# Performance work log

Measured on AMD Instinct MI355X. Metric: run time of the kernel, lower is better.

Reference implementation:

```python
import jax, jax.numpy as jnp
import numpy as np

MIN_NORM = 1e-15
EPS = 1e-7
MASK_FILL = -9e15


def logmap0(x, c):
    # Hyperboloid log map at the origin (HGCN convention, K = 1/c)
    K = 1.0 / c
    sqrtK = K ** 0.5
    y = x[:, 1:]
    y_norm = jnp.clip(jnp.linalg.norm(y, axis=-1, keepdims=True), MIN_NORM)
    theta = jnp.clip(x[:, :1] / sqrtK, 1.0 + EPS)
    res = sqrtK * jnp.arccosh(theta) * y / y_norm
    return jnp.concatenate([jnp.zeros_like(x[:, :1]), res], axis=1)


def proj(x, c):
    # normalize: recompute time coordinate so x lies on the hyperboloid
    K = 1.0 / c
    y = x[:, 1:]
    x0 = jnp.sqrt(K + jnp.sum(y * y, axis=-1, keepdims=True))
    return jnp.concatenate([x0, y], axis=1)


def expmap0(u, c):
    K = 1.0 / c
    sqrtK = K ** 0.5
    x = u[:, 1:]
    x_norm = jnp.clip(jnp.linalg.norm(x, axis=-1, keepdims=True), MIN_NORM)
    theta = x_norm / sqrtK
    res = jnp.concatenate(
        [sqrtK * jnp.cosh(theta), sqrtK * jnp.sinh(theta) * x / x_norm], axis=1
    )
    return proj(res, c)


def setup_inputs() -> dict:
    key = jax.random.key(0)
    k1, k2, k3, k4, k5 = jax.random.split(key, 5)
    N, D_in, D_out = 8192, 256, 256
    x = jax.random.normal(k1, (N, D_in), dtype=jnp.float32)
    adj = jax.random.randint(k2, (N, N), 0, 2, dtype=jnp.int32)
    W_gcn = jax.random.normal(k3, (D_in - 1, D_out - 1), dtype=jnp.float32)
    # xavier_uniform-like scale (gain=1.414)
    std_w = 1.414 * (2.0 / (D_out + D_out)) ** 0.5
    W_att = jax.random.normal(k4, (D_out, D_out), dtype=jnp.float32) * std_w
    std_a = 1.414 * (2.0 / (2 * D_out + 1)) ** 0.5
    a_att = jax.random.normal(k5, (2 * D_out, 1), dtype=jnp.float32) * std_a
    return {"x": x, "adj": adj, "k": 1, "W_gcn": W_gcn, "W_att": W_att, "a_att": a_att}


def reference(x, adj, k, W_gcn, W_att, a_att):
    c = float(k)  # curvature
    N = x.shape[0]
    # tangent-space linear map, keeping time coordinate zero
    logx = logmap0(x, c)
    Wx = logx[:, 1:] @ W_gcn  # [N, D_out-1]
    tmp = jnp.concatenate([jnp.zeros((N, 1), x.dtype), Wx], axis=1)
    fun7 = proj(expmap0(tmp, c), c)  # expmap0 + normalize
    h_in = logmap0(fun7, c)  # [N, D_out]
    # GraphAttentionLayer (dense GAT; a_input @ a decomposes into rank-1 terms)
    h = h_in @ W_att  # [N, F]
    F_ = h.shape[1]
    e = (h @ a_att[:F_]) + (h @ a_att[F_:]).T  # [N, N]; == cat([h_i, h_j]) @ a
    att = jnp.where(adj > 0, e, MASK_FILL)
    att = jax.nn.softmax(att, axis=1)  # dropout omitted (eval mode)
    h_prime = att @ h
    emb = jax.nn.elu(h_prime)  # concat=True
    emb = proj(emb, c)  # manifold.normalize
    # HypAct with sigmoid
    out = expmap0(jax.nn.sigmoid(logmap0(emb, c)), c)
    return out
```

## Files before the change

kernel.cpp:

```cpp
#include <hip/hip_runtime.h>
#include <hip/hip_bf16.h>
#include <math.h>

typedef __attribute__((ext_vector_type(4))) float f32x4;
typedef __attribute__((ext_vector_type(8))) short bf16x8;
typedef __attribute__((ext_vector_type(2))) unsigned long long u64x2;

#define N_ROWS 8192
#define D 256
#define MSHIFT 16.0f
#define NKB 8
#define KRANGE (N_ROWS / NKB)
#define NSTEP (KRANGE / 32)

__device__ __forceinline__ unsigned short f2bf(float f) {
    unsigned int u = __float_as_uint(f);
    unsigned int r = u + 0x7FFFu + ((u >> 16) & 1u);
    return (unsigned short)(r >> 16);
}
__device__ __forceinline__ float bf2f(unsigned short h) {
    return __uint_as_float(((unsigned int)h) << 16);
}

__device__ __forceinline__ float breduce_sum256(float v, float* sb) {
#pragma unroll
    for (int off = 32; off; off >>= 1) v += __shfl_down(v, off);
    int wid = threadIdx.x >> 6;
    __syncthreads();
    if ((threadIdx.x & 63) == 0) sb[wid] = v;
    __syncthreads();
    return sb[0] + sb[1] + sb[2] + sb[3];
}

__device__ __forceinline__ void dma16(const void* g, void* l) {
    __builtin_amdgcn_global_load_lds(
        (const __attribute__((address_space(1))) unsigned int*)g,
        (__attribute__((address_space(3))) unsigned int*)l, 16, 0, 0);
}

__device__ __forceinline__ bf16x8 bits2bf(unsigned int w32, int sh) {
    unsigned int m = w32 >> sh;
    bf16x8 r;
#pragma unroll
    for (int j = 0; j < 8; ++j)
        r[j] = (m & (1u << j)) ? (short)0x3F80 : (short)0;
    return r;
}

__global__ void __launch_bounds__(512)
k_pack(const int* __restrict__ adj, const float* __restrict__ wexp,
       unsigned long long* __restrict__ pack64, float* __restrict__ rowsum) {
    __shared__ float wlds[N_ROWS];
    const int tid = threadIdx.x;
    const int l = tid & 63;
    const int row = blockIdx.x * 8 + (tid >> 6);
#pragma unroll
    for (int i = 0; i < 4; ++i) {
        float4 v4 = *(const float4*)(wexp + (i * 512 + tid) * 4);
        *(float4*)(&wlds[(i * 512 + tid) * 4]) = v4;
    }
    __syncthreads();

    const int* arow = adj + (size_t)row * N_ROWS;
    float rs = 0.f;
    for (int g = 0; g < 8; ++g) {
        int a[16];
#pragma unroll
        for (int i = 0; i < 16; ++i) a[i] = arow[(g * 16 + i) * 64 + l];
        __builtin_amdgcn_sched_barrier(0);
        unsigned long long m[16];
#pragma unroll
        for (int i = 0; i < 16; ++i) {
            m[i] = __ballot(a[i] != 0);
            rs += a[i] ? wlds[(g * 16 + i) * 64 + l] : 0.f;
        }
        if (l == 0) {
#pragma unroll
            for (int i = 0; i < 8; ++i) {
                u64x2 st = {m[2 * i], m[2 * i + 1]};
                *(u64x2*)(&pack64[(size_t)row * 128 + g * 16 + 2 * i]) = st;
            }
        }
    }
#pragma unroll
    for (int off = 32; off; off >>= 1) rs += __shfl_xor(rs, off);
    if (l == 0) rowsum[row] = rs;
}

__global__ void k_M2v(const float* __restrict__ Wg, const float* __restrict__ Wa,
                      const float* __restrict__ aatt,
                      unsigned short* __restrict__ M2Thi, unsigned short* __restrict__ M2Tlo,
                      float* __restrict__ v) {
    __shared__ float sb[4];
    int k = blockIdx.x, t = threadIdx.x;
    float acc = 0.f;
#pragma unroll 8
    for (int m = 0; m < 255; ++m)
        acc += Wg[k * 255 + m] * Wa[(m + 1) * 256 + t];
    unsigned short hi = f2bf(acc);
    unsigned short lo = f2bf(acc - bf2f(hi));
    M2Thi[t * 256 + k] = hi;
    M2Tlo[t * 256 + k] = lo;
    if (k == 0) { M2Thi[t * 256 + 255] = 0; M2Tlo[t * 256 + 255] = 0; }
    float s = breduce_sum256(acc * aatt[256 + t], sb);
    if (t == 0) v[k] = s;
}

__global__ void k_logw(const float* __restrict__ x, const float* __restrict__ v,
                       float* __restrict__ wexp,
                       unsigned short* __restrict__ Awhi, unsigned short* __restrict__ Awlo) {
    __shared__ float sb[4];
    int i0 = blockIdx.x * 8, t = threadIdx.x;
    float vv = (t >= 1) ? v[t - 1] : 0.f;
#pragma unroll
    for (int r = 0; r < 8; ++r) {
        float xv = x[(size_t)(i0 + r) * D + t];
        float yv = (t >= 1) ? xv : 0.f;
        float ss = breduce_sum256(yv * yv, sb);
        float x0 = x[(size_t)(i0 + r) * D];
        float coef = acoshf(fmaxf(x0, 1.f + 1e-7f)) / fmaxf(sqrtf(ss), 1e-15f);
        float lg = coef * yv;
        float c = breduce_sum256(lg * vv, sb);
        float w = expf(c - MSHIFT);
        if (t == r) wexp[i0 + r] = w;
        float aw = w * lg;
        unsigned short hi = f2bf(aw);
        unsigned short lo = f2bf(aw - bf2f(hi));
        int kd = (t == 0) ? 255 : (t - 1);
        Awhi[(size_t)(i0 + r) * 256 + kd] = hi;
        Awlo[(size_t)(i0 + r) * 256 + kd] = lo;
    }
}

__global__ void __launch_bounds__(512)
k_hGT(const unsigned short* __restrict__ M2Thi, const unsigned short* __restrict__ M2Tlo,
      const unsigned short* __restrict__ Awhi, const unsigned short* __restrict__ Awlo,
      unsigned short* __restrict__ GT) {
    __shared__ __align__(16) char ahi[32768], alo[32768], bhi[8192], blo[8192];
    const int tid = threadIdx.x;
    const int w = tid >> 6, l = tid & 63;
    const int lr = l & 15, lq = l >> 4;
    const int i0 = blockIdx.x * 64;
    const int gs = (l & 7) ^ (l >> 3);

    const unsigned short* srcAhi[4];
    const unsigned short* srcAlo[4];
#pragma unroll
    for (int i = 0; i < 4; ++i) {
        int rowA = (w * 4 + i) * 8 + (l >> 3);
        srcAhi[i] = M2Thi + rowA * 256 + gs * 8;
        srcAlo[i] = M2Tlo + rowA * 256 + gs * 8;
    }
    int rowB = w * 8 + (l >> 3);
    const unsigned short* srcBhi = Awhi + (size_t)(i0 + rowB) * 256 + gs * 8;
    const unsigned short* srcBlo = Awlo + (size_t)(i0 + rowB) * 256 + gs * 8;

    f32x4 zero4 = {0.f, 0.f, 0.f, 0.f};
    f32x4 acc[2][4];
#pragma unroll
    for (int m = 0; m < 2; ++m)
#pragma unroll
        for (int n = 0; n < 4; ++n) acc[m][n] = zero4;

    for (int t = 0; t < 4; ++t) {
        if (t) __syncthreads();
#pragma unroll
        for (int i = 0; i < 4; ++i) {
            dma16(srcAhi[i] + t * 64, ahi + (w * 4 + i) * 1024);
            dma16(srcAlo[i] + t * 64, alo + (w * 4 + i) * 1024);
        }
        dma16(srcBhi + t * 64, bhi + w * 1024);
        dma16(srcBlo + t * 64, blo + w * 1024);
        asm volatile("s_waitcnt vmcnt(0)" ::: "memory");
        __syncthreads();
#pragma unroll
        for (int ks = 0; ks < 2; ++ks) {
            const int g = ((ks * 4 + lq) ^ (lr & 7)) * 16;
            bf16x8 afh[2], afl[2];
#pragma unroll
            for (int m = 0; m < 2; ++m) {
                int row = w * 32 + m * 16 + lr;
                afh[m] = *(const bf16x8*)(ahi + row * 128 + g);
                afl[m] = *(const bf16x8*)(alo + row * 128 + g);
            }
#pragma unroll
            for (int n = 0; n < 4; ++n) {
                int rb = n * 16 + lr;
                bf16x8 bfh = *(const bf16x8*)(bhi + rb * 128 + g);
                bf16x8 bfl = *(const bf16x8*)(blo + rb * 128 + g);
#pragma unroll
                for (int m = 0; m < 2; ++m) {
                    acc[m][n] = __builtin_amdgcn_mfma_f32_16x16x32_bf16(afh[m], bfh, acc[m][n], 0, 0, 0);
                    acc[m][n] = __builtin_amdgcn_mfma_f32_16x16x32_bf16(afh[m], bfl, acc[m][n], 0, 0, 0);
                    acc[m][n] = __builtin_amdgcn_mfma_f32_16x16x32_bf16(afl[m], bfh, acc[m][n], 0, 0, 0);
                }
            }
        }
    }
#pragma unroll
    for (int m = 0; m < 2; ++m)
#pragma unroll
        for (int n = 0; n < 4; ++n)
#pragma unroll
            for (int vv = 0; vv < 4; ++vv) {
                int c = w * 32 + m * 16 + lq * 4 + vv;
                GT[(size_t)c * N_ROWS + i0 + n * 16 + lr] = f2bf(acc[m][n][vv]);
            }
}

__global__ void __launch_bounds__(512)
k_attbits(const unsigned int* __restrict__ pack32, const unsigned short* __restrict__ GT,
          float* __restrict__ part) {
    __shared__ __align__(16) unsigned int bitlds[256 * 36];
    __shared__ __align__(16) char bufB[3][16384];
    const int tid = threadIdx.x;
    const int kb = blockIdx.x & 7;
    const int rb = blockIdx.x >> 3;
    const int i0 = rb * 256;
    const int kbeg = kb * KRANGE;
    const int w = tid >> 6, l = tid & 63;
    const int lr = l & 15, lq = l >> 4;
    const int wm = w >> 1, wn = w & 1;

    {
        const int rloc = tid >> 3, gb = tid & 7;
#pragma unroll
        for (int p = 0; p < 4; ++p) {
            uint4 vb = *(const uint4*)(pack32 + (size_t)(i0 + p * 64 + rloc) * 256 + kb * 32 + gb * 4);
            *(uint4*)(bitlds + (p * 64 + rloc) * 36 + gb * 4) = vb;
        }
    }

    const int col4 = l >> 2, gB = ((l & 3) ^ (col4 & 3)) * 8;
    const unsigned short* srcB[2];
#pragma unroll
    for (int i = 0; i < 2; ++i) {
        int b = w * 2 + i;
        srcB[i] = GT + (size_t)(b * 16 + col4) * N_ROWS + kbeg + gB;
    }
#define STAGEB(T_, BI_) do {                                           \
        _Pragma("unroll")                                              \
        for (int i_ = 0; i_ < 2; ++i_)                                 \
            dma16(srcB[i_] + (T_) * 32, bufB[BI_] + (w * 2 + i_) * 1024); \
    } while (0)

    f32x4 zero4 = {0.f, 0.f, 0.f, 0.f};
    f32x4 acc[4][8];
#pragma unroll
    for (int m = 0; m < 4; ++m)
#pragma unroll
        for (int n = 0; n < 8; ++n) acc[m][n] = zero4;

    STAGEB(0, 0);
    STAGEB(1, 1);
    __syncthreads();

    int cb = 0;
    for (int t = 0; t < NSTEP; ++t) {
        if (t > 0) {
            if (t < NSTEP - 1) asm volatile("s_waitcnt vmcnt(2)" ::: "memory");
            else               asm volatile("s_waitcnt vmcnt(0)" ::: "memory");
            __builtin_amdgcn_sched_barrier(0);
            __builtin_amdgcn_s_barrier();
            __builtin_amdgcn_sched_barrier(0);
        }
        if (t + 2 < NSTEP) {
            int nb2 = (cb >= 1) ? cb - 1 : cb + 2;
            STAGEB(t + 2, nb2);
        }
        const char* bB = bufB[cb];

        bf16x8 af[4];
#pragma unroll
        for (int m = 0; m < 4; ++m) {
            int row = wm * 64 + m * 16 + lr;
            unsigned int bits = bitlds[row * 36 + t];
            af[m] = bits2bf(bits, lq * 8);
        }
#pragma unroll
        for (int n = 0; n < 8; ++n) {
            int col = wn * 128 + n * 16 + lr;
            bf16x8 bf = *(const bf16x8*)(bB + col * 64 + ((lq ^ (lr & 3)) << 4));
#pragma unroll
            for (int m = 0; m < 4; ++m)
                acc[m][n] = __builtin_amdgcn_mfma_f32_16x16x32_bf16(af[m], bf, acc[m][n], 0, 0, 0);
        }
        cb = (cb == 2) ? 0 : cb + 1;
    }
#undef STAGEB

    float* pbase = part + (size_t)kb * N_ROWS * D;
#pragma unroll
    for (int m = 0; m < 4; ++m)
#pragma unroll
        for (int n = 0; n < 8; ++n) {
            int orow = i0 + wm * 64 + m * 16 + lq * 4;
            int ocol = wn * 128 + n * 16 + lr;
            float* op = pbase + (size_t)orow * D + ocol;
#pragma unroll
            for (int vv = 0; vv < 4; ++vv)
                __builtin_nontemporal_store(acc[m][n][vv], op + (size_t)vv * D);
        }
}

__global__ void k_final3(const float* __restrict__ part, const float* __restrict__ rowsum,
                         float* __restrict__ out) {
    __shared__ float sb[4];
    int row = blockIdx.x, t = threadIdx.x;
    float raw = 0.f;
#pragma unroll
    for (int kbi = 0; kbi < NKB; ++kbi)
        raw += __builtin_nontemporal_load(&part[((size_t)kbi * N_ROWS + row) * D + t]);
    float rs = rowsum[row];
    float hp = raw / rs;
    float ey = 0.f;
    if (t >= 1) ey = (hp > 0.f) ? hp : expm1f(hp);
    float ss = breduce_sum256(ey * ey, sb);
    float x0 = sqrtf(1.f + ss);
    float th = fmaxf(x0, 1.f + 1e-7f);
    float al = acoshf(th);
    float yn = fmaxf(sqrtf(ss), 1e-15f);
    float u = (t >= 1) ? (al * ey / yn) : 0.f;
    float s = 1.f / (1.f + expf(-u));
    float s2 = (t >= 1) ? s * s : 0.f;
    float ssn = breduce_sum256(s2, sb);
    float xn = fmaxf(sqrtf(ssn), 1e-15f);
    float sh = sinhf(xn);
    float yf = (t >= 1) ? (sh * s / xn) : 0.f;
    float sy = breduce_sum256(yf * yf, sb);
    float res = (t == 0) ? sqrtf(1.f + sy) : yf;
    out[(size_t)row * D + t] = res;
}

extern "C" void kernel_launch(void* const* d_in, const int* in_sizes, int n_in,
                              void* d_out, int out_size, void* d_ws, size_t ws_size,
                              hipStream_t stream) {
    const float* x    = (const float*)d_in[0];
    const int*   adj  = (const int*)d_in[1];
    const float* Wg   = (const float*)d_in[3];
    const float* Wa   = (const float*)d_in[4];
    const float* aatt = (const float*)d_in[5];
    float* out = (float*)d_out;

    char* wsb = (char*)d_ws;
    unsigned short* M2Thi  = (unsigned short*)(wsb);
    unsigned short* M2Tlo  = (unsigned short*)(wsb + 0x0020000);
    float*          v      = (float*)(wsb + 0x0040000);
    float*          wexp   = (float*)(wsb + 0x0048000);
    float*          rowsum = (float*)(wsb + 0x0050000);
    unsigned short* Awhi   = (unsigned short*)(wsb + 0x0100000);
    unsigned short* Awlo   = (unsigned short*)(wsb + 0x0500000);
    unsigned short* GT     = (unsigned short*)(wsb + 0x0900000);
    float*          part   = (float*)(wsb + 0x1000000);
    unsigned long long* pack64 = (unsigned long long*)(wsb + 0x5000000);

    k_M2v<<<255, 256, 0, stream>>>(Wg, Wa, aatt, M2Thi, M2Tlo, v);
    k_logw<<<N_ROWS / 8, 256, 0, stream>>>(x, v, wexp, Awhi, Awlo);
    k_pack<<<N_ROWS / 8, 512, 0, stream>>>(adj, wexp, pack64, rowsum);
    k_hGT<<<N_ROWS / 64, 512, 0, stream>>>(M2Thi, M2Tlo, Awhi, Awlo, GT);
    k_attbits<<<32 * NKB, 512, 0, stream>>>((const unsigned int*)pack64, GT, part);
    k_final3<<<N_ROWS, 256, 0, stream>>>(part, rowsum, out);
}
```

Before: 183.6 us.

## Vectorize adjacency packing with int4 loads and double-buffered row prefetch

The adjacency bit-packing kernel now has each wave cover a 1024-column slice of all 8 rows, loading int4 vectors instead of scalar ints. The next row is double-buffered so its load overlaps the current row's work. Bitmasks are built by nibble-shifting and OR-reducing with shuffles instead of ballots, and per-row sums go through a small LDS reduction. This aims to cut instruction count and raise memory throughput on the 256 MB adjacency read, at the cost of extra shuffles and a block barrier.

```diff
diff --git a/kernel.cpp b/kernel.cpp
--- a/kernel.cpp
+++ b/kernel.cpp
@@ -4,7 +4,6 @@
 
 typedef __attribute__((ext_vector_type(4))) float f32x4;
 typedef __attribute__((ext_vector_type(8))) short bf16x8;
-typedef __attribute__((ext_vector_type(2))) unsigned long long u64x2;
 
 #define N_ROWS 8192
 #define D 256
@@ -51,9 +50,10 @@
 k_pack(const int* __restrict__ adj, const float* __restrict__ wexp,
        unsigned long long* __restrict__ pack64, float* __restrict__ rowsum) {
     __shared__ float wlds[N_ROWS];
+    __shared__ float rsred[8][8];
     const int tid = threadIdx.x;
-    const int l = tid & 63;
-    const int row = blockIdx.x * 8 + (tid >> 6);
+    const int w = tid >> 6, l = tid & 63;
+    const int row0 = blockIdx.x * 8;
 #pragma unroll
     for (int i = 0; i < 4; ++i) {
         float4 v4 = *(const float4*)(wexp + (i * 512 + tid) * 4);
@@ -61,30 +61,49 @@
     }
     __syncthreads();
 
-    const int* arow = adj + (size_t)row * N_ROWS;
-    float rs = 0.f;
-    for (int g = 0; g < 8; ++g) {
-        int a[16];
-#pragma unroll
-        for (int i = 0; i < 16; ++i) a[i] = arow[(g * 16 + i) * 64 + l];
+    const size_t koff = (size_t)w * 1024 + l * 4;
+    const int* base = adj + (size_t)row0 * N_ROWS + koff;
+    int4 abuf[2][4];
+#pragma unroll
+    for (int i = 0; i < 4; ++i)
+        abuf[0][i] = *(const int4*)(base + i * 256);
+
+    for (int r = 0; r < 8; ++r) {
+        if (r + 1 < 8) {
+#pragma unroll
+            for (int i = 0; i < 4; ++i)
+                abuf[(r + 1) & 1][i] = *(const int4*)(base + (size_t)(r + 1) * N_ROWS + i * 256);
+        }
         __builtin_amdgcn_sched_barrier(0);
-        unsigned long long m[16];
-#pragma unroll
-        for (int i = 0; i < 16; ++i) {
-            m[i] = __ballot(a[i] != 0);
-            rs += a[i] ? wlds[(g * 16 + i) * 64 + l] : 0.f;
-        }
-        if (l == 0) {
-#pragma unroll
-            for (int i = 0; i < 8; ++i) {
-                u64x2 st = {m[2 * i], m[2 * i + 1]};
-                *(u64x2*)(&pack64[(size_t)row * 128 + g * 16 + 2 * i]) = st;
-            }
-        }
-    }
-#pragma unroll
-    for (int off = 32; off; off >>= 1) rs += __shfl_xor(rs, off);
-    if (l == 0) rowsum[row] = rs;
+        const int4* A = abuf[r & 1];
+        float rs = 0.f;
+#pragma unroll
+        for (int i = 0; i < 4; ++i) {
+            int4 a = A[i];
+            float4 wv = *(const float4*)(&wlds[w * 1024 + i * 256 + l * 4]);
+            unsigned int nb = (a.x ? 1u : 0u) | (a.y ? 2u : 0u) |
+                              (a.z ? 4u : 0u) | (a.w ? 8u : 0u);
+            unsigned long long v = (unsigned long long)nb << (4 * (l & 15));
+            rs += (a.x ? wv.x : 0.f) + (a.y ? wv.y : 0.f) +
+                  (a.z ? wv.z : 0.f) + (a.w ? wv.w : 0.f);
+            v |= __shfl_xor(v, 1);
+            v |= __shfl_xor(v, 2);
+            v |= __shfl_xor(v, 4);
+            v |= __shfl_xor(v, 8);
+            if ((l & 15) == 0)
+                pack64[(size_t)(row0 + r) * 128 + w * 16 + i * 4 + (l >> 4)] = v;
+        }
+#pragma unroll
+        for (int off = 32; off; off >>= 1) rs += __shfl_xor(rs, off);
+        if (l == 0) rsred[r][w] = rs;
+    }
+    __syncthreads();
+    if (tid < 8) {
+        float s = 0.f;
+#pragma unroll
+        for (int j = 0; j < 8; ++j) s += rsred[tid][j];
+        rowsum[row0 + tid] = s;
+    }
 }
 
 __global__ void k_M2v(const float* __restrict__ Wg, const float* __restrict__ Wa,
```

Result: faster. 178.6 us (-2.7%).
